# Kernel optimization log

Measured on AMD Instinct MI355X. Metric: run time of the kernel, lower is better.

The kernel has to match this reference:

```python
import jax, jax.numpy as jnp
import numpy as np

B, C, H, W = 4, 256, 64, 64
DQ = C // 8

def setup_inputs() -> dict:
    key = jax.random.key(0)
    ks = jax.random.split(key, 7)
    x = jax.random.normal(ks[0], (B, C, H, W), dtype=jnp.float32)
    # 1x1 convs == per-pixel linear layers: weight [out, in], bias [out]
    Wq = jax.random.normal(ks[1], (DQ, C), dtype=jnp.float32) * (1.0 / np.sqrt(C))
    bq = jax.random.normal(ks[2], (DQ,), dtype=jnp.float32) * 0.01
    Wk = jax.random.normal(ks[3], (DQ, C), dtype=jnp.float32) * (1.0 / np.sqrt(C))
    bk = jax.random.normal(ks[4], (DQ,), dtype=jnp.float32) * 0.01
    Wv = jax.random.normal(ks[5], (C, C), dtype=jnp.float32) * (1.0 / np.sqrt(C))
    bv = jax.random.normal(ks[6], (C,), dtype=jnp.float32) * 0.01
    return {"x": x, "Wq": Wq, "bq": bq, "Wk": Wk, "bk": bk, "Wv": Wv, "bv": bv}

def reference(x, Wq, bq, Wk, bk, Wv, bv):
    b, c, h, w = x.shape
    n = h * w
    xf = x.reshape(b, c, n)                                  # [b,c,n]
    Q = jnp.einsum('dc,bcn->bnd', Wq, xf) + bq               # [b,n,dq]
    K = jnp.einsum('dc,bcn->bdn', Wk, xf) + bk[None, :, None]  # [b,dq,n]
    A = jax.nn.softmax(jnp.einsum('bnd,bdm->bnm', Q, K), axis=-1)  # [b,n,n]
    V = jnp.einsum('oc,bcn->bon', Wv, xf) + bv[None, :, None]      # [b,c,n]
    # torch: bmm(V, A^T) -> out[b,c,i] = sum_j V[b,c,j] * A[b,i,j]
    out = jnp.einsum('bcj,bij->bci', V, A)
    return x + out.reshape(b, c, h, w)
```

## Files before the change

### kernel.cpp

```cpp
#include <hip/hip_runtime.h>
#include <math.h>

#define BB 4
#define CC 256
#define NN 4096
#define DQ 32
#define LOG2E 1.44269504f

typedef _Float16 half8 __attribute__((ext_vector_type(8)));
typedef _Float16 half4 __attribute__((ext_vector_type(4)));
typedef float float4v __attribute__((ext_vector_type(4)));

__global__ __launch_bounds__(64) void prep_kernel(
    const float* __restrict__ Wq, const float* __restrict__ bq,
    const float* __restrict__ Wk, const float* __restrict__ bk,
    const float* __restrict__ Wv, const float* __restrict__ bv,
    _Float16* __restrict__ Wh, float* __restrict__ bh)
{
    int o = blockIdx.x, t = threadIdx.x;
    const float* src; float scale = 1.0f, bias;
    if (o < DQ)            { src = Wq + o * CC;        scale = LOG2E; bias = bq[o] * LOG2E; }
    else if (o < 2 * DQ)   { src = Wk + (o - DQ) * CC;                bias = bk[o - DQ]; }
    else                   { src = Wv + (o - 2 * DQ) * CC;            bias = bv[o - 2 * DQ]; }
    float4 v = *(const float4*)(src + t * 4);
    half4 h = { (_Float16)(v.x * scale), (_Float16)(v.y * scale),
                (_Float16)(v.z * scale), (_Float16)(v.w * scale) };
    *(half4*)(Wh + o * CC + t * 4) = h;
    if (t == 0) bh[o] = bias;
}

__global__ __launch_bounds__(256) void proj_kernel(
    const float* __restrict__ x, const _Float16* __restrict__ Wh,
    const float* __restrict__ bh,
    _Float16* __restrict__ Qt, _Float16* __restrict__ Kt,
    _Float16* __restrict__ Vh)
{
    __shared__ _Float16 xl[32 * 256];
    __shared__ _Float16 os_qk[32 * 72];
    __shared__ _Float16 os_v[256 * 40];

    const int tid = threadIdx.x;
    const int lane = tid & 63, w = tid >> 6;
    const int i16 = lane & 15, q = lane >> 4;
    const int n0 = blockIdx.x * 32, b = blockIdx.y;

    const float* xb = x + (size_t)b * CC * NN + n0;
    #pragma unroll
    for (int u = 0; u < 8; ++u) {
        int idx = u * 256 + tid;
        int c = idx >> 3, n4 = idx & 7;
        float4 v = *(const float4*)(xb + (size_t)c * NN + n4 * 4);
        int chunk = c >> 3, cl = c & 7;
        float vv[4] = {v.x, v.y, v.z, v.w};
        #pragma unroll
        for (int e = 0; e < 4; ++e) {
            int n = n4 * 4 + e;
            xl[n * 256 + ((chunk ^ n) * 8) + cl] = (_Float16)vv[e];
        }
    }

    float4v acc[5][2];
    const int obase = 80 * w;
    #pragma unroll
    for (int ot = 0; ot < 5; ++ot) {
        float4 b4 = *(const float4*)(bh + obase + 16 * ot + 4 * q);
        #pragma unroll
        for (int nt = 0; nt < 2; ++nt)
            acc[ot][nt] = (float4v){b4.x, b4.y, b4.z, b4.w};
    }
    __syncthreads();

    #pragma unroll
    for (int k = 0; k < 8; ++k) {
        half8 af[5], bf[2];
        #pragma unroll
        for (int ot = 0; ot < 5; ++ot)
            af[ot] = *(const half8*)(Wh + (size_t)(obase + 16 * ot + i16) * CC + k * 32 + 8 * q);
        #pragma unroll
        for (int nt = 0; nt < 2; ++nt) {
            int n = 16 * nt + i16;
            bf[nt] = *(const half8*)&xl[n * 256 + (((4 * k + q) ^ n) * 8)];
        }
        #pragma unroll
        for (int ot = 0; ot < 5; ++ot)
            #pragma unroll
            for (int nt = 0; nt < 2; ++nt)
                acc[ot][nt] = __builtin_amdgcn_mfma_f32_16x16x32_f16(af[ot], bf[nt], acc[ot][nt], 0, 0, 0);
    }

    #pragma unroll
    for (int ot = 0; ot < 5; ++ot) {
        int og = obase + 16 * ot;
        #pragma unroll
        for (int nt = 0; nt < 2; ++nt) {
            int n = 16 * nt + i16;
            if (og < 64) {
                half4 hv = { (_Float16)acc[ot][nt][0], (_Float16)acc[ot][nt][1],
                             (_Float16)acc[ot][nt][2], (_Float16)acc[ot][nt][3] };
                *(half4*)&os_qk[n * 72 + og + 4 * q] = hv;
            } else {
                int cb = og - 64 + 4 * q;
                #pragma unroll
                for (int r = 0; r < 4; ++r)
                    os_v[(cb + r) * 40 + n] = (_Float16)acc[ot][nt][r];
            }
        }
    }
    __syncthreads();

    _Float16* Qtb = Qt + (size_t)b * NN * DQ;
    _Float16* Ktb = Kt + (size_t)b * NN * DQ;
    {
        int n = tid >> 3, p = tid & 7;
        half8 hv = *(const half8*)&os_qk[n * 72 + 8 * p];
        if (p < 4) *(half8*)(Qtb + (size_t)(n0 + n) * DQ + 8 * p) = hv;
        else       *(half8*)(Ktb + (size_t)(n0 + n) * DQ + 8 * (p - 4)) = hv;
    }
    _Float16* Vb = Vh + (size_t)b * CC * NN;
    #pragma unroll
    for (int u = 0; u < 4; ++u) {
        int c = u * 64 + (tid >> 2), p = tid & 3;
        half8 hv = *(const half8*)&os_v[c * 40 + 8 * p];
        *(half8*)(Vb + (size_t)c * NN + n0 + 8 * p) = hv;
    }
}

__global__ __launch_bounds__(256) void attn_kernel(
    const float* __restrict__ x,
    const _Float16* __restrict__ Qt, const _Float16* __restrict__ Kt,
    const _Float16* __restrict__ Vh,
    float* __restrict__ out)
{
    __shared__ _Float16 k2[2][64 * 32];
    __shared__ _Float16 ps2[2][32 * 72];
    __shared__ float    stx[4][32];

    const int tid = threadIdx.x;
    const int w = tid >> 6, lane = tid & 63;
    const int i16 = lane & 15, q = lane >> 4;
    const int i0 = blockIdx.x * 32, b = blockIdx.y;

    const _Float16* Ktb = Kt + (size_t)b * NN * DQ;
    const _Float16* Vb  = Vh + (size_t)b * CC * NN;

    half8 qb[2];
    {
        const _Float16* Qtb = Qt + (size_t)b * NN * DQ;
        qb[0] = *(const half8*)(Qtb + (size_t)(i0 + i16) * DQ + 8 * q);
        qb[1] = *(const half8*)(Qtb + (size_t)(i0 + 16 + i16) * DQ + 8 * q);
    }

    float mA[2] = {-INFINITY, -INFINITY};
    {
        const _Float16* kq = Ktb + (size_t)(1024 * w) * DQ;
        half8 kf[4];
        #pragma unroll
        for (int u = 0; u < 4; ++u)
            kf[u] = *(const half8*)(kq + (size_t)(16 * u + i16) * DQ + 8 * q);
        for (int t = 0; t < 64; t += 4) {
            #pragma unroll
            for (int u = 0; u < 4; ++u) {
                half8 ka = kf[u];
                int nt = t + 4 + u;
                if (nt < 64)
                    kf[u] = *(const half8*)(kq + (size_t)(16 * nt + i16) * DQ + 8 * q);
                float4v z = {0.f, 0.f, 0.f, 0.f};
                float4v s0 = __builtin_amdgcn_mfma_f32_16x16x32_f16(ka, qb[0], z, 0, 0, 0);
                float4v s1 = __builtin_amdgcn_mfma_f32_16x16x32_f16(ka, qb[1], z, 0, 0, 0);
                mA[0] = fmaxf(mA[0], fmaxf(fmaxf(s0[0], s0[1]), fmaxf(s0[2], s0[3])));
                mA[1] = fmaxf(mA[1], fmaxf(fmaxf(s1[0], s1[1]), fmaxf(s1[2], s1[3])));
            }
        }
        #pragma unroll
        for (int it = 0; it < 2; ++it) {
            mA[it] = fmaxf(mA[it], __shfl_xor(mA[it], 16, 64));
            mA[it] = fmaxf(mA[it], __shfl_xor(mA[it], 32, 64));
        }
        if (q == 0) { stx[w][i16] = mA[0]; stx[w][16 + i16] = mA[1]; }
    }
    __syncthreads();

    float m2v[2];
    #pragma unroll
    for (int it = 0; it < 2; ++it) {
        int r = 16 * it + i16;
        m2v[it] = fmaxf(fmaxf(stx[0][r], stx[1][r]), fmaxf(stx[2][r], stx[3][r]));
    }

    float4v O[4][2];
    #pragma unroll
    for (int ct = 0; ct < 4; ++ct)
        #pragma unroll
        for (int it = 0; it < 2; ++it)
            O[ct][it] = (float4v){0.f, 0.f, 0.f, 0.f};
    float lB[2] = {0.f, 0.f};

    const int jK = tid >> 2, dgK = tid & 3;
    const int kaddr = jK * 32 + ((dgK ^ (jK & 3)) * 8);
    const int jS = 16 * w + i16;
    const int ka_off = jS * 32 + ((q ^ (jS & 3)) * 8);

    const _Float16* vp[8];
    #pragma unroll
    for (int ct = 0; ct < 4; ++ct)
        #pragma unroll
        for (int ks = 0; ks < 2; ++ks)
            vp[ct * 2 + ks] = Vb + (size_t)(64 * w + 16 * ct + i16) * NN + 32 * ks + 8 * q;

    half8 kv;
    kv = *(const half8*)(Ktb + (size_t)jK * DQ + 8 * dgK);
    *(half8*)&k2[0][kaddr] = kv;
    kv = *(const half8*)(Ktb + (size_t)(64 + jK) * DQ + 8 * dgK);

    half8 vbA[8], vbB[8];

    auto stageK = [&](int t) {
        if (t < 63) *(half8*)&k2[(t + 1) & 1][kaddr] = kv;
        if (t < 62) kv = *(const half8*)(Ktb + (size_t)((t + 2) * 64 + jK) * DQ + 8 * dgK);
    };
    auto loadV = [&](half8* dst, int t) {
        #pragma unroll
        for (int u = 0; u < 8; ++u)
            dst[u] = *(const half8*)(vp[u] + 64 * t);
    };
    auto pvPhase = [&](const half8* va, const _Float16* psp) {
        half8 pb[2][2];
        #pragma unroll
        for (int ks = 0; ks < 2; ++ks)
            #pragma unroll
            for (int it = 0; it < 2; ++it)
                pb[ks][it] = *(const half8*)&psp[(16 * it + i16) * 72 + 32 * ks + 8 * q];
        __builtin_amdgcn_s_setprio(1);
        #pragma unroll
        for (int ct = 0; ct < 4; ++ct)
            #pragma unroll
            for (int ks = 0; ks < 2; ++ks)
                #pragma unroll
                for (int it = 0; it < 2; ++it)
                    O[ct][it] = __builtin_amdgcn_mfma_f32_16x16x32_f16(va[ct * 2 + ks], pb[ks][it], O[ct][it], 0, 0, 0);
        __builtin_amdgcn_s_setprio(0);
    };
    auto sPhase = [&](int t) {
        half8 ka = *(const half8*)&k2[t & 1][ka_off];
        _Float16* psc = ps2[t & 1];
        #pragma unroll
        for (int it = 0; it < 2; ++it) {
            float4v z = {0.f, 0.f, 0.f, 0.f};
            float4v s = __builtin_amdgcn_mfma_f32_16x16x32_f16(ka, qb[it], z, 0, 0, 0);
            float p0 = exp2f(s[0] - m2v[it]);
            float p1 = exp2f(s[1] - m2v[it]);
            float p2 = exp2f(s[2] - m2v[it]);
            float p3 = exp2f(s[3] - m2v[it]);
            lB[it] += (p0 + p1) + (p2 + p3);
            half4 hv = { (_Float16)p0, (_Float16)p1, (_Float16)p2, (_Float16)p3 };
            *(half4*)&psc[(16 * it + i16) * 72 + 16 * w + 4 * q] = hv;
        }
    };

    for (int tt = 0; tt < 64; tt += 2) {
        __syncthreads();
        stageK(tt);
        loadV(vbA, tt);
        if (tt > 0) pvPhase(vbB, ps2[1]);
        sPhase(tt);
        __syncthreads();
        stageK(tt + 1);
        loadV(vbB, tt + 1);
        pvPhase(vbA, ps2[0]);
        sPhase(tt + 1);
    }
    __syncthreads();
    pvPhase(vbB, ps2[1]);

    #pragma unroll
    for (int it = 0; it < 2; ++it) {
        lB[it] += __shfl_xor(lB[it], 16, 64);
        lB[it] += __shfl_xor(lB[it], 32, 64);
    }
    if (q == 0) { stx[w][i16] = lB[0]; stx[w][16 + i16] = lB[1]; }
    __syncthreads();
    float linv[2];
    #pragma unroll
    for (int it = 0; it < 2; ++it) {
        int r = 16 * it + i16;
        linv[it] = 1.0f / ((stx[0][r] + stx[1][r]) + (stx[2][r] + stx[3][r]));
    }

    const float* xb = x + (size_t)b * CC * NN;
    float* ob = out + (size_t)b * CC * NN;
    #pragma unroll
    for (int ct = 0; ct < 4; ++ct)
        #pragma unroll
        for (int it = 0; it < 2; ++it)
            #pragma unroll
            for (int r = 0; r < 4; ++r) {
                int c = 64 * w + 16 * ct + 4 * q + r;
                size_t idx = (size_t)c * NN + i0 + 16 * it + i16;
                ob[idx] = xb[idx] + O[ct][it][r] * linv[it];
            }
}

extern "C" void kernel_launch(void* const* d_in, const int* in_sizes, int n_in,
                              void* d_out, int out_size, void* d_ws, size_t ws_size,
                              hipStream_t stream) {
    const float* x  = (const float*)d_in[0];
    const float* Wq = (const float*)d_in[1];
    const float* bq = (const float*)d_in[2];
    const float* Wk = (const float*)d_in[3];
    const float* bk = (const float*)d_in[4];
    const float* Wv = (const float*)d_in[5];
    const float* bv = (const float*)d_in[6];
    float* out = (float*)d_out;

    char* ws = (char*)d_ws;
    _Float16* Wh = (_Float16*)(ws);
    float*    bh = (float*)(ws + 163840);
    _Float16* Qt = (_Float16*)(ws + 262144);
    _Float16* Kt = (_Float16*)(ws + 1310720);
    _Float16* Vh = (_Float16*)(ws + 2359296);

    prep_kernel<<<dim3(320), 64, 0, stream>>>(Wq, bq, Wk, bk, Wv, bv, Wh, bh);
    proj_kernel<<<dim3(NN / 32, BB), 256, 0, stream>>>(x, Wh, bh, Qt, Kt, Vh);
    attn_kernel<<<dim3(NN / 32, BB), 256, 0, stream>>>(x, Qt, Kt, Vh, out);
}
```

Measured before the change: 216.3 us.

## Make each wave compute full score tiles independently, removing block barriers

The attention main loop no longer splits the score computation across waves through shared LDS tiles. Each wave now loads K from global itself, computes all 64 keys' scores for its 32 queries, and writes P into a private swizzled LDS region, so no __syncthreads is needed in the loop and the row sum reduces inside the wave. The cost is that the QK^T MFMAs and exp2f work are done four times per block (once per wave), plus more K global loads and register pressure. The max prepass K prefetch depth also goes from 4 to 8.

```diff
diff --git a/kernel.cpp b/kernel.cpp
--- a/kernel.cpp
+++ b/kernel.cpp
@@ -131,14 +131,14 @@
     const _Float16* __restrict__ Vh,
     float* __restrict__ out)
 {
-    __shared__ _Float16 k2[2][64 * 32];
-    __shared__ _Float16 ps2[2][32 * 72];
+    __shared__ _Float16 Pp[4][32 * 64];
     __shared__ float    stx[4][32];
 
     const int tid = threadIdx.x;
     const int w = tid >> 6, lane = tid & 63;
     const int i16 = lane & 15, q = lane >> 4;
     const int i0 = blockIdx.x * 32, b = blockIdx.y;
+    const int sw = i16 & 7;
 
     const _Float16* Ktb = Kt + (size_t)b * NN * DQ;
     const _Float16* Vb  = Vh + (size_t)b * CC * NN;
@@ -153,15 +153,15 @@
     float mA[2] = {-INFINITY, -INFINITY};
     {
         const _Float16* kq = Ktb + (size_t)(1024 * w) * DQ;
-        half8 kf[4];
-        #pragma unroll
-        for (int u = 0; u < 4; ++u)
+        half8 kf[8];
+        #pragma unroll
+        for (int u = 0; u < 8; ++u)
             kf[u] = *(const half8*)(kq + (size_t)(16 * u + i16) * DQ + 8 * q);
-        for (int t = 0; t < 64; t += 4) {
-            #pragma unroll
-            for (int u = 0; u < 4; ++u) {
+        for (int t = 0; t < 64; t += 8) {
+            #pragma unroll
+            for (int u = 0; u < 8; ++u) {
                 half8 ka = kf[u];
-                int nt = t + 4 + u;
+                int nt = t + 8 + u;
                 if (nt < 64)
                     kf[u] = *(const half8*)(kq + (size_t)(16 * nt + i16) * DQ + 8 * q);
                 float4v z = {0.f, 0.f, 0.f, 0.f};
@@ -195,10 +195,7 @@
             O[ct][it] = (float4v){0.f, 0.f, 0.f, 0.f};
     float lB[2] = {0.f, 0.f};
 
-    const int jK = tid >> 2, dgK = tid & 3;
-    const int kaddr = jK * 32 + ((dgK ^ (jK & 3)) * 8);
-    const int jS = 16 * w + i16;
-    const int ka_off = jS * 32 + ((q ^ (jS & 3)) * 8);
+    _Float16* myP = &Pp[w][0];
 
     const _Float16* vp[8];
     #pragma unroll
@@ -207,29 +204,38 @@
         for (int ks = 0; ks < 2; ++ks)
             vp[ct * 2 + ks] = Vb + (size_t)(64 * w + 16 * ct + i16) * NN + 32 * ks + 8 * q;
 
-    half8 kv;
-    kv = *(const half8*)(Ktb + (size_t)jK * DQ + 8 * dgK);
-    *(half8*)&k2[0][kaddr] = kv;
-    kv = *(const half8*)(Ktb + (size_t)(64 + jK) * DQ + 8 * dgK);
-
-    half8 vbA[8], vbB[8];
-
-    auto stageK = [&](int t) {
-        if (t < 63) *(half8*)&k2[(t + 1) & 1][kaddr] = kv;
-        if (t < 62) kv = *(const half8*)(Ktb + (size_t)((t + 2) * 64 + jK) * DQ + 8 * dgK);
-    };
     auto loadV = [&](half8* dst, int t) {
         #pragma unroll
         for (int u = 0; u < 8; ++u)
             dst[u] = *(const half8*)(vp[u] + 64 * t);
     };
-    auto pvPhase = [&](const half8* va, const _Float16* psp) {
+    auto loadK = [&](half8* dst, int t) {
+        #pragma unroll
+        for (int s = 0; s < 4; ++s)
+            dst[s] = *(const half8*)(Ktb + (size_t)(64 * t + 16 * s + i16) * DQ + 8 * q);
+    };
+    auto tile = [&](const half8* va, const half8* kf) {
+        #pragma unroll
+        for (int s = 0; s < 4; ++s) {
+            #pragma unroll
+            for (int it = 0; it < 2; ++it) {
+                float4v z = {0.f, 0.f, 0.f, 0.f};
+                float4v sv = __builtin_amdgcn_mfma_f32_16x16x32_f16(kf[s], qb[it], z, 0, 0, 0);
+                float p0 = exp2f(sv[0] - m2v[it]);
+                float p1 = exp2f(sv[1] - m2v[it]);
+                float p2 = exp2f(sv[2] - m2v[it]);
+                float p3 = exp2f(sv[3] - m2v[it]);
+                lB[it] += (p0 + p1) + (p2 + p3);
+                half4 hv = { (_Float16)p0, (_Float16)p1, (_Float16)p2, (_Float16)p3 };
+                *(half4*)(myP + (16 * it + i16) * 64 + (((2 * s + (q >> 1)) ^ sw) * 8) + (q & 1) * 4) = hv;
+            }
+        }
         half8 pb[2][2];
         #pragma unroll
         for (int ks = 0; ks < 2; ++ks)
             #pragma unroll
             for (int it = 0; it < 2; ++it)
-                pb[ks][it] = *(const half8*)&psp[(16 * it + i16) * 72 + 32 * ks + 8 * q];
+                pb[ks][it] = *(const half8*)(myP + (16 * it + i16) * 64 + (((4 * ks + q) ^ sw) * 8));
         __builtin_amdgcn_s_setprio(1);
         #pragma unroll
         for (int ct = 0; ct < 4; ++ct)
@@ -240,50 +246,24 @@
                     O[ct][it] = __builtin_amdgcn_mfma_f32_16x16x32_f16(va[ct * 2 + ks], pb[ks][it], O[ct][it], 0, 0, 0);
         __builtin_amdgcn_s_setprio(0);
     };
-    auto sPhase = [&](int t) {
-        half8 ka = *(const half8*)&k2[t & 1][ka_off];
-        _Float16* psc = ps2[t & 1];
-        #pragma unroll
-        for (int it = 0; it < 2; ++it) {
-            float4v z = {0.f, 0.f, 0.f, 0.f};
-            float4v s = __builtin_amdgcn_mfma_f32_16x16x32_f16(ka, qb[it], z, 0, 0, 0);
-            float p0 = exp2f(s[0] - m2v[it]);
-            float p1 = exp2f(s[1] - m2v[it]);
-            float p2 = exp2f(s[2] - m2v[it]);
-            float p3 = exp2f(s[3] - m2v[it]);
-            lB[it] += (p0 + p1) + (p2 + p3);
-            half4 hv = { (_Float16)p0, (_Float16)p1, (_Float16)p2, (_Float16)p3 };
-            *(half4*)&psc[(16 * it + i16) * 72 + 16 * w + 4 * q] = hv;
-        }
-    };
+
+    half8 vA[8], vB[8], kA[4], kB[4];
+    loadV(vA, 0); loadK(kA, 0);
+    loadV(vB, 1); loadK(kB, 1);
 
     for (int tt = 0; tt < 64; tt += 2) {
-        __syncthreads();
-        stageK(tt);
-        loadV(vbA, tt);
-        if (tt > 0) pvPhase(vbB, ps2[1]);
-        sPhase(tt);
-        __syncthreads();
-        stageK(tt + 1);
-        loadV(vbB, tt + 1);
-        pvPhase(vbA, ps2[0]);
-        sPhase(tt + 1);
-    }
-    __syncthreads();
-    pvPhase(vbB, ps2[1]);
-
+        tile(vA, kA);
+        if (tt + 2 < 64) { loadV(vA, tt + 2); loadK(kA, tt + 2); }
+        tile(vB, kB);
+        if (tt + 3 < 64) { loadV(vB, tt + 3); loadK(kB, tt + 3); }
+    }
+
+    float linv[2];
     #pragma unroll
     for (int it = 0; it < 2; ++it) {
         lB[it] += __shfl_xor(lB[it], 16, 64);
         lB[it] += __shfl_xor(lB[it], 32, 64);
-    }
-    if (q == 0) { stx[w][i16] = lB[0]; stx[w][16 + i16] = lB[1]; }
-    __syncthreads();
-    float linv[2];
-    #pragma unroll
-    for (int it = 0; it < 2; ++it) {
-        int r = 16 * it + i16;
-        linv[it] = 1.0f / ((stx[0][r] + stx[1][r]) + (stx[2][r] + stx[3][r]));
+        linv[it] = 1.0f / lB[it];
     }
 
     const float* xb = x + (size_t)b * CC * NN;
```

Measured after the change: 258.8 us. +19.6%, slower.
